# Optimization experiments

Hardware: AMD Instinct MI355X
Metric: run time of the kernel (lower is better)

Reference implementation:

```python
import jax, jax.numpy as jnp
import numpy as np
from jax import lax

C = 128
KS = 9
PAD = KS // 2


def _conv1d(r, w):
    # r: [B, C, L], w: [Cout, Cin, K] -> [B, C, L], SAME padding
    return lax.conv_general_dilated(r, w, window_strides=(1,), padding=[(PAD, PAD)],
                                    dimension_numbers=("NCH", "OIH", "NCH"))


def _pass_once(x, w, vertical, reverse):
    # x: [B, C, H, W]; scan sequentially along H (vertical) or W (horizontal).
    if not vertical:
        x = jnp.transpose(x, (0, 1, 3, 2))  # scan axis -> axis 2
    if reverse:
        x = jnp.flip(x, axis=2)
    xs = jnp.moveaxis(x, 2, 0)  # [S, B, C, L]

    def step(carry, xi):
        y = xi + jax.nn.relu(_conv1d(carry, w))
        return y, y

    _, ys = lax.scan(step, xs[0], xs[1:])
    out = jnp.concatenate([xs[:1], ys], axis=0)
    out = jnp.moveaxis(out, 0, 2)
    if reverse:
        out = jnp.flip(out, axis=2)
    if not vertical:
        out = jnp.transpose(out, (0, 1, 3, 2))
    return out


def setup_inputs() -> dict:
    key = jax.random.key(0)
    kx, k1, k2, k3, k4 = jax.random.split(key, 5)
    B, H, W = 8, 128, 256
    std = (1.0 / (C * KS)) ** 0.5  # kaiming_normal_(a=1) scale
    x = jax.random.normal(kx, (B, C, H, W), dtype=jnp.float32)
    w_ud = jax.random.normal(k1, (C, C, KS), dtype=jnp.float32) * std
    w_du = jax.random.normal(k2, (C, C, KS), dtype=jnp.float32) * std
    w_lr = jax.random.normal(k3, (C, C, KS), dtype=jnp.float32) * std
    w_rl = jax.random.normal(k4, (C, C, KS), dtype=jnp.float32) * std
    return {"x": x, "w_ud": w_ud, "w_du": w_du, "w_lr": w_lr, "w_rl": w_rl}


def reference(x, w_ud, w_du, w_lr, w_rl):
    # Order matches torch ModuleList: up_down, down_up, left_right, right_left
    x = _pass_once(x, w_ud, vertical=True, reverse=False)
    x = _pass_once(x, w_du, vertical=True, reverse=True)
    x = _pass_once(x, w_lr, vertical=False, reverse=False)
    x = _pass_once(x, w_rl, vertical=False, reverse=True)
    return x
```

## Files before the change

kernel.cpp:

```cpp
#include <hip/hip_runtime.h>

#define C_ 128
#define KS_ 9
#define B_ 8
#define H_ 128
#define W_ 256
#define HW_ (H_ * W_)
#define CHW_ (C_ * HW_)

typedef _Float16 half8 __attribute__((ext_vector_type(8)));
typedef float floatx4 __attribute__((ext_vector_type(4)));
typedef unsigned long long ull;

#define F16_IMG_BYTES 67108864u

#define WS_WF_OFF    0u
#define WS_WF_BYTES  1179648u
#define WS_CARRY_OFF 1183744u
#define CARRY_HALVES (8 * 256 * 128)
#define WS_YT_OFF    2232320u
#define WS_NEED      (WS_YT_OFF + F16_IMG_BYTES)

__device__ __forceinline__ int imin(int a, int b) { return a < b ? a : b; }
__device__ __forceinline__ int imax(int a, int b) { return a > b ? a : b; }

__global__ void k_copy(const float* __restrict__ in, float* __restrict__ out, int n4) {
  int i = blockIdx.x * blockDim.x + threadIdx.x;
  int stride = gridDim.x * blockDim.x;
  const floatx4* ip = (const floatx4*)in;
  floatx4* op = (floatx4*)out;
  for (; i < n4; i += stride) op[i] = ip[i];
}

__global__ void k_wprep(const float* w0, const float* w1, const float* w2, const float* w3,
                        _Float16* __restrict__ wf) {
  const float* Wp[4] = {w0, w1, w2, w3};
  const float* W = Wp[blockIdx.y];
  _Float16* out = wf + (size_t)blockIdx.y * (8 * 36 * 64 * 8);
  int idx = blockIdx.x * 256 + threadIdx.x;
  if (idx >= 8 * 36 * 64 * 8) return;
  int j = idx & 7;
  int lane = (idx >> 3) & 63;
  int ks = (idx >> 9) % 36;
  int mt = (idx >> 9) / 36;
  int co = mt * 16 + (lane & 15);
  int k = ks * 32 + ((lane >> 4) & 3) * 8 + j;
  int kk = k >> 7, ci = k & 127;
  out[idx] = (_Float16)W[((size_t)co * C_ + ci) * KS_ + kk];
}

template <typename XT, typename YT>
__global__ void k_carry0(const XT* __restrict__ imgX, YT* __restrict__ imgY,
                         _Float16* __restrict__ cout_, int S, int L, int istart) {
  int b = blockIdx.y;
  int e = blockIdx.x * 256 + threadIdx.x;
  if (e >= L * 16) return;
  int col = e >> 4, ci0 = (e & 15) * 8;
  union { ull u[2]; _Float16 h[8]; } pk;
#pragma unroll
  for (int u2 = 0; u2 < 8; ++u2) {
    size_t off = ((size_t)(b * C_ + ci0 + u2) * S + istart) * L + col;
    float v = (float)imgX[off];
    pk.h[u2] = (_Float16)v;
    imgY[off] = (YT)v;
  }
  ull* dst = (ull*)(cout_ + ((size_t)b * L + col) * 128 + ci0);
  dst[0] = pk.u[0];
  dst[1] = pk.u[1];
}

__global__ void k_t1h(const _Float16* __restrict__ in, _Float16* __restrict__ out) {
  __shared__ _Float16 tile[32][33];
  size_t pbase = (size_t)blockIdx.z * HW_;
  int h0 = blockIdx.y * 32, w0 = blockIdx.x * 32;
  int tx = threadIdx.x, ty = threadIdx.y;
  for (int i = 0; i < 32; i += 8)
    tile[ty + i][tx] = in[pbase + (size_t)(h0 + ty + i) * W_ + (w0 + tx)];
  __syncthreads();
  for (int i = 0; i < 32; i += 8)
    out[pbase + (size_t)(w0 + ty + i) * H_ + (h0 + tx)] = tile[tx][ty + i];
}

__global__ void k_t2(const _Float16* __restrict__ in, float* __restrict__ out) {
  __shared__ float tile[32][33];
  size_t pbase = (size_t)blockIdx.z * HW_;
  int h0 = blockIdx.y * 32, w0 = blockIdx.x * 32;
  int tx = threadIdx.x, ty = threadIdx.y;
  for (int i = 0; i < 32; i += 8)
    tile[ty + i][tx] = (float)in[pbase + (size_t)(w0 + ty + i) * H_ + (h0 + tx)];
  __syncthreads();
  for (int i = 0; i < 32; i += 8)
    out[pbase + (size_t)(h0 + ty + i) * W_ + (w0 + tx)] = tile[tx][ty + i];
}

template <typename XT, typename YT, int WC, int MAXT>
__global__ __launch_bounds__(512, 2) void k_scan3(
    const XT* __restrict__ imgX, YT* __restrict__ imgY,
    const _Float16* __restrict__ Wf, const _Float16* __restrict__ cin,
    _Float16* __restrict__ cout_,
    int S, int L, int n0, int nsteps, int dir, int istart) {
  constexpr int MAXW = WC + 72;
  constexpr int BSZ = MAXW * 132;
  __shared__ _Float16 Bl[2][BSZ];
  __shared__ floatx4 Sc[2][8][64];
  const int c0 = blockIdx.x * WC;
  const int b = blockIdx.y;
  const int t = threadIdx.x;
  const int lane = t & 63, wave = t >> 6;
  const int q = lane >> 4, m = lane & 15;
  const int h = wave & 1;
  const int g = wave >> 1;

  half8 A0[18], A1[18];
  {
    const half8* wp2 = (const half8*)Wf;
#pragma unroll
    for (int i = 0; i < 18; ++i) {
      A0[i] = wp2[((g * 2 + 0) * 36 + h * 18 + i) * 64 + lane];
      A1[i] = wp2[((g * 2 + 1) * 36 + h * 18 + i) * 64 + lane];
    }
  }

  for (int i = t * 8; i < BSZ; i += 4096) {
    ull* z0 = (ull*)(&Bl[0][i]);
    ull* z1 = (ull*)(&Bl[1][i]);
    z0[0] = 0ull; z0[1] = 0ull;
    z1[0] = 0ull; z1[1] = 0ull;
  }
  __syncthreads();

  {
    const int NCH = (WC + 64) * 16;
    for (int e = t; e < NCH; e += 512) {
      const int lcol = e >> 4;
      const int col = c0 - 32 + lcol;
      if (col >= 0 && col < L) {
        const int ci0 = (e & 15) * 8;
        const ull* src = (const ull*)(cin + ((size_t)b * L + col) * 128 + ci0);
        ull* dst = (ull*)(&Bl[0][(lcol + 4) * 132 + ci0]);
        dst[0] = src[0];
        dst[1] = src[1];
      }
    }
  }
  __syncthreads();

  int cur = 0;
  for (int p = 1; p <= nsteps; ++p) {
    const int row = istart + dir * (n0 + p);
    const int ext = 32 - 4 * p;
    const int lo = imax(c0 - ext, 0);
    const int hi = imin(c0 + WC + ext, L);
    const int tt0 = -((c0 - lo + 15) >> 4);
    const int ntile = ((hi - c0 + 15) >> 4) - tt0;
    const _Float16* BR = Bl[cur];
    _Float16* BW = Bl[cur ^ 1];
    const size_t rbase = ((size_t)(b * C_ + wave * 16) * S + row) * L;

    float xv[MAXT][4];
#pragma unroll
    for (int u = 0; u < MAXT; ++u) {
      if (u >= ntile) break;
      const int col = c0 + (tt0 + u) * 16 + m;
      const bool ld2 = (col >= lo) && (col < hi);
#pragma unroll
      for (int r = 0; r < 4; ++r)
        xv[u][r] = ld2 ? (float)imgX[rbase + (size_t)(q * 4 + r) * (S * L) + col] : 0.f;
    }

#pragma unroll
    for (int u = 0; u < MAXT; ++u) {
      if (u >= ntile) break;
      const int ti = tt0 + u;
      floatx4 aA = {0.f, 0.f, 0.f, 0.f}, aB = {0.f, 0.f, 0.f, 0.f};
      const int lbase = ti * 16 + m + 32;
#pragma unroll
      for (int i = 0; i < 18; ++i) {
        const int ks = h * 18 + i;
        const int kk = ks >> 2;
        const int ci0 = (ks & 3) * 32 + q * 8;
        const ull* bp = (const ull*)(BR + (lbase + kk) * 132 + ci0);
        union { ull u2[2]; half8 v; } bf;
        bf.u2[0] = bp[0]; bf.u2[1] = bp[1];
        aA = __builtin_amdgcn_mfma_f32_16x16x32_f16(A0[i], bf.v, aA, 0, 0, 0);
        aB = __builtin_amdgcn_mfma_f32_16x16x32_f16(A1[i], bf.v, aB, 0, 0, 0);
      }
      Sc[u & 1][wave][lane] = h ? aA : aB;
      __syncthreads();
      const floatx4 ac = (h ? aB : aA) + Sc[u & 1][wave ^ 1][lane];
      const int col = c0 + ti * 16 + m;
      const bool instrip = (col >= c0) && (col < c0 + WC);
      const bool inlds = (col >= lo) && (col < hi);
      union { ull uu; _Float16 h4[4]; } pk;
#pragma unroll
      for (int r = 0; r < 4; ++r) {
        const float y = xv[u][r] + fmaxf(ac[r], 0.f);
        pk.h4[r] = (_Float16)y;
        if (instrip)
          imgY[rbase + (size_t)(q * 4 + r) * (S * L) + col] = (YT)y;
      }
      if (inlds)
        *(ull*)(BW + (col - c0 + 36) * 132 + wave * 16 + q * 4) = pk.uu;
    }
    __syncthreads();
    cur ^= 1;
  }

  {
    const _Float16* BP = Bl[cur];
    for (int e = t; e < WC * 16; e += 512) {
      const int lc = e >> 4, ci0 = (e & 15) * 8;
      ull* dst = (ull*)(cout_ + ((size_t)b * L + (c0 + lc)) * 128 + ci0);
      const ull* src = (const ull*)(BP + (lc + 36) * 132 + ci0);
      dst[0] = src[0];
      dst[1] = src[1];
    }
  }
}

__device__ __forceinline__ void gemm_acc_fb(const _Float16* Bl, const _Float16* __restrict__ Wfrag,
                                            int wrow_base, int lane, floatx4* acc) {
  const int q = lane >> 4;
  const half8* wfp = (const half8*)Wfrag + lane;
  for (int ks = 0; ks < 36; ++ks) {
    int k0 = ks * 32 + q * 8;
    int kk = k0 >> 7;
    int ci0 = k0 & 127;
    half8 bf = *(const half8*)&Bl[(size_t)(wrow_base + kk) * C_ + ci0];
    const half8* wp = wfp + ks * 64;
#pragma unroll
    for (int mt = 0; mt < 8; ++mt)
      acc[mt] = __builtin_amdgcn_mfma_f32_16x16x32_f16(wp[mt * 36 * 64], bf, acc[mt], 0, 0, 0);
  }
}

__global__ __launch_bounds__(256) void k_step_v(float* __restrict__ Y,
                                                const _Float16* __restrict__ Wfrag,
                                                int row, int prev) {
  __shared__ _Float16 Bl[80 * 128];
  const int b = blockIdx.y, w0 = blockIdx.x * 64, t = threadIdx.x;
  {
    const float* base = Y + (size_t)b * CHW_ + (size_t)prev * W_;
#pragma unroll
    for (int it = 0; it < 10; ++it) {
      int c = it * 256 + t;
      int ci = c / 20, c4 = c % 20;
      int wst = w0 - 8 + c4 * 4;
      const float* p = base + (size_t)ci * HW_ + wst;
      float v[4];
      if (wst >= 0 && wst + 4 <= W_) {
        floatx4 u = *(const floatx4*)p;
        v[0] = u[0]; v[1] = u[1]; v[2] = u[2]; v[3] = u[3];
      } else {
#pragma unroll
        for (int j = 0; j < 4; ++j) { int w = wst + j; v[j] = (w >= 0 && w < W_) ? p[j] : 0.f; }
      }
      int wl = c4 * 4;
#pragma unroll
      for (int j = 0; j < 4; ++j) Bl[(wl + j) * C_ + ci] = (_Float16)v[j];
    }
  }
  __syncthreads();
  const int lane = t & 63, wave = t >> 6, q = lane >> 4, l15 = lane & 15;
  floatx4 acc[8];
#pragma unroll
  for (int mt = 0; mt < 8; ++mt) acc[mt] = (floatx4){0.f, 0.f, 0.f, 0.f};
  gemm_acc_fb(Bl, Wfrag, wave * 16 + l15 + 4, lane, acc);
  const int wcol = w0 + wave * 16 + l15;
#pragma unroll
  for (int mt = 0; mt < 8; ++mt)
#pragma unroll
    for (int r = 0; r < 4; ++r) {
      int co = mt * 16 + q * 4 + r;
      size_t off = (size_t)b * CHW_ + (size_t)co * HW_ + (size_t)row * W_ + wcol;
      Y[off] = Y[off] + fmaxf(acc[mt][r], 0.f);
    }
}

__global__ __launch_bounds__(256) void k_step_h(float* __restrict__ Y,
                                                const _Float16* __restrict__ Wfrag,
                                                int row, int prev) {
  __shared__ _Float16 Bl[80 * 128];
  const int b = blockIdx.y, h0 = blockIdx.x * 64, t = threadIdx.x;
  {
    const float* base = Y + (size_t)b * CHW_ + prev;
    for (int e = t; e < 80 * 128; e += 256) {
      int hl = e >> 7, ci = e & 127, h = h0 - 8 + hl;
      float v = 0.f;
      if (h >= 0 && h < H_) v = base[(size_t)ci * HW_ + (size_t)h * W_];
      Bl[hl * C_ + ci] = (_Float16)v;
    }
  }
  __syncthreads();
  const int lane = t & 63, wave = t >> 6, q = lane >> 4, l15 = lane & 15;
  floatx4 acc[8];
#pragma unroll
  for (int mt = 0; mt < 8; ++mt) acc[mt] = (floatx4){0.f, 0.f, 0.f, 0.f};
  gemm_acc_fb(Bl, Wfrag, wave * 16 + l15 + 4, lane, acc);
  const int hc = h0 + wave * 16 + l15;
#pragma unroll
  for (int mt = 0; mt < 8; ++mt)
#pragma unroll
    for (int r = 0; r < 4; ++r) {
      int co = mt * 16 + q * 4 + r;
      size_t off = (size_t)b * CHW_ + (size_t)co * HW_ + (size_t)hc * W_ + row;
      Y[off] = Y[off] + fmaxf(acc[mt][r], 0.f);
    }
}

extern "C" void kernel_launch(void* const* d_in, const int* in_sizes, int n_in,
                              void* d_out, int out_size, void* d_ws, size_t ws_size,
                              hipStream_t stream) {
  const float* x = (const float*)d_in[0];
  const float* w_ud = (const float*)d_in[1];
  const float* w_du = (const float*)d_in[2];
  const float* w_lr = (const float*)d_in[3];
  const float* w_rl = (const float*)d_in[4];

  float* Y = (float*)d_out;
  char* ws = (char*)d_ws;
  _Float16* Wf = (_Float16*)(ws + WS_WF_OFF);
  _Float16* carryA = (_Float16*)(ws + WS_CARRY_OFF);
  _Float16* carryB = carryA + CARRY_HALVES;
  _Float16* YtA = (_Float16*)(ws + WS_YT_OFF);
  _Float16* F16A = (_Float16*)d_out;
  _Float16* F16B = (_Float16*)((char*)d_out + F16_IMG_BYTES);

  const size_t WF_PASS = 8 * 36 * 64 * 8;

  k_wprep<<<dim3(576, 4), 256, 0, stream>>>(w_ud, w_du, w_lr, w_rl, Wf);

  if (ws_size >= WS_NEED) {
    _Float16* cb_[2] = {carryA, carryB};
    k_carry0<float, float><<<dim3(16, B_), 256, 0, stream>>>(x, Y, carryA, H_, W_, 0);
    for (int n0 = 0, j = 0; n0 < H_ - 1; n0 += 8, ++j) {
      int ns = H_ - 1 - n0; if (ns > 8) ns = 8;
      k_scan3<float, float, 8, 5><<<dim3(32, B_), 512, 0, stream>>>(
          x, Y, Wf + 0 * WF_PASS, cb_[j & 1], cb_[(j + 1) & 1], H_, W_, n0, ns, +1, 0);
    }
    k_carry0<float, _Float16><<<dim3(16, B_), 256, 0, stream>>>(Y, YtA, carryA, H_, W_, H_ - 1);
    for (int n0 = 0, j = 0; n0 < H_ - 1; n0 += 8, ++j) {
      int ns = H_ - 1 - n0; if (ns > 8) ns = 8;
      k_scan3<float, _Float16, 8, 5><<<dim3(32, B_), 512, 0, stream>>>(
          Y, YtA, Wf + 1 * WF_PASS, cb_[j & 1], cb_[(j + 1) & 1], H_, W_, n0, ns, -1, H_ - 1);
    }
    k_t1h<<<dim3(8, 4, B_ * C_), dim3(32, 8), 0, stream>>>(YtA, F16A);
    k_carry0<_Float16, _Float16><<<dim3(8, B_), 256, 0, stream>>>(F16A, YtA, carryA, W_, H_, 0);
    for (int n0 = 0, j = 0; n0 < W_ - 1; n0 += 8, ++j) {
      int ns = W_ - 1 - n0; if (ns > 8) ns = 8;
      k_scan3<_Float16, _Float16, 4, 5><<<dim3(32, B_), 512, 0, stream>>>(
          F16A, YtA, Wf + 2 * WF_PASS, cb_[j & 1], cb_[(j + 1) & 1], W_, H_, n0, ns, +1, 0);
    }
    k_carry0<_Float16, _Float16><<<dim3(8, B_), 256, 0, stream>>>(YtA, F16B, carryA, W_, H_, W_ - 1);
    for (int n0 = 0, j = 0; n0 < W_ - 1; n0 += 8, ++j) {
      int ns = W_ - 1 - n0; if (ns > 8) ns = 8;
      k_scan3<_Float16, _Float16, 4, 5><<<dim3(32, B_), 512, 0, stream>>>(
          YtA, F16B, Wf + 3 * WF_PASS, cb_[j & 1], cb_[(j + 1) & 1], W_, H_, n0, ns, -1, W_ - 1);
    }
    k_copy<<<2048, 256, 0, stream>>>((const float*)F16B, (float*)YtA, F16_IMG_BYTES / 16);
    k_t2<<<dim3(8, 4, B_ * C_), dim3(32, 8), 0, stream>>>(YtA, Y);
  } else {
    k_copy<<<2048, 256, 0, stream>>>(x, Y, B_ * C_ * H_ * W_ / 4);
    for (int i = 1; i < H_; ++i)
      k_step_v<<<dim3(W_ / 64, B_), 256, 0, stream>>>(Y, Wf + 0 * WF_PASS, i, i - 1);
    for (int i = H_ - 2; i >= 0; --i)
      k_step_v<<<dim3(W_ / 64, B_), 256, 0, stream>>>(Y, Wf + 1 * WF_PASS, i, i + 1);
    for (int i = 1; i < W_; ++i)
      k_step_h<<<dim3(H_ / 64, B_), 256, 0, stream>>>(Y, Wf + 2 * WF_PASS, i, i - 1);
    for (int i = W_ - 2; i >= 0; --i)
      k_step_h<<<dim3(H_ / 64, B_), 256, 0, stream>>>(Y, Wf + 3 * WF_PASS, i, i + 1);
  }
}
```

Baseline: 4.215 ms.

## Single-buffer LDS carry, batch tile syncs, prefetch next row inputs

The scan kernel moves from double-buffered LDS to a single buffer, with the row stride padded to 136. All MFMA tiles are computed before one barrier instead of syncing per tile, so the cross-wave partial sums now need one scratch slot per tile. The next row's x values are loaded before the end-of-step barrier so the global load latency overlaps the sync. MAXT drops to 4 for the horizontal passes to cut register and LDS use. The single buffer depends on every read finishing before the barrier that precedes the writes.

```diff
diff --git a/kernel.cpp b/kernel.cpp
--- a/kernel.cpp
+++ b/kernel.cpp
@@ -100,9 +100,9 @@
     _Float16* __restrict__ cout_,
     int S, int L, int n0, int nsteps, int dir, int istart) {
   constexpr int MAXW = WC + 72;
-  constexpr int BSZ = MAXW * 132;
-  __shared__ _Float16 Bl[2][BSZ];
-  __shared__ floatx4 Sc[2][8][64];
+  constexpr int BSZ = MAXW * 136;
+  __shared__ _Float16 Bl[BSZ];
+  __shared__ floatx4 Sc[MAXT][8][64];
   const int c0 = blockIdx.x * WC;
   const int b = blockIdx.y;
   const int t = threadIdx.x;
@@ -122,10 +122,9 @@
   }
 
   for (int i = t * 8; i < BSZ; i += 4096) {
-    ull* z0 = (ull*)(&Bl[0][i]);
-    ull* z1 = (ull*)(&Bl[1][i]);
-    z0[0] = 0ull; z0[1] = 0ull;
-    z1[0] = 0ull; z1[1] = 0ull;
+    ull* z = (ull*)(&Bl[i]);
+    z[0] = 0ull;
+    z[1] = 0ull;
   }
   __syncthreads();
 
@@ -137,27 +136,24 @@
       if (col >= 0 && col < L) {
         const int ci0 = (e & 15) * 8;
         const ull* src = (const ull*)(cin + ((size_t)b * L + col) * 128 + ci0);
-        ull* dst = (ull*)(&Bl[0][(lcol + 4) * 132 + ci0]);
+        ull* dst = (ull*)(&Bl[(lcol + 4) * 136 + ci0]);
         dst[0] = src[0];
         dst[1] = src[1];
       }
     }
   }
-  __syncthreads();
-
-  int cur = 0;
-  for (int p = 1; p <= nsteps; ++p) {
-    const int row = istart + dir * (n0 + p);
-    const int ext = 32 - 4 * p;
-    const int lo = imax(c0 - ext, 0);
-    const int hi = imin(c0 + WC + ext, L);
-    const int tt0 = -((c0 - lo + 15) >> 4);
-    const int ntile = ((hi - c0 + 15) >> 4) - tt0;
-    const _Float16* BR = Bl[cur];
-    _Float16* BW = Bl[cur ^ 1];
-    const size_t rbase = ((size_t)(b * C_ + wave * 16) * S + row) * L;
-
-    float xv[MAXT][4];
+
+  int row, lo, hi, tt0, ntile;
+  size_t rbase;
+  float xv[MAXT][4];
+  {
+    row = istart + dir * (n0 + 1);
+    const int ext = 32 - 4;
+    lo = imax(c0 - ext, 0);
+    hi = imin(c0 + WC + ext, L);
+    tt0 = -((c0 - lo + 15) >> 4);
+    ntile = ((hi - c0 + 15) >> 4) - tt0;
+    rbase = ((size_t)(b * C_ + wave * 16) * S + row) * L;
 #pragma unroll
     for (int u = 0; u < MAXT; ++u) {
       if (u >= ntile) break;
@@ -167,7 +163,11 @@
       for (int r = 0; r < 4; ++r)
         xv[u][r] = ld2 ? (float)imgX[rbase + (size_t)(q * 4 + r) * (S * L) + col] : 0.f;
     }
-
+  }
+  __syncthreads();
+
+  for (int p = 1; p <= nsteps; ++p) {
+    floatx4 xa[MAXT];
 #pragma unroll
     for (int u = 0; u < MAXT; ++u) {
       if (u >= ntile) break;
@@ -179,15 +179,20 @@
         const int ks = h * 18 + i;
         const int kk = ks >> 2;
         const int ci0 = (ks & 3) * 32 + q * 8;
-        const ull* bp = (const ull*)(BR + (lbase + kk) * 132 + ci0);
-        union { ull u2[2]; half8 v; } bf;
-        bf.u2[0] = bp[0]; bf.u2[1] = bp[1];
-        aA = __builtin_amdgcn_mfma_f32_16x16x32_f16(A0[i], bf.v, aA, 0, 0, 0);
-        aB = __builtin_amdgcn_mfma_f32_16x16x32_f16(A1[i], bf.v, aB, 0, 0, 0);
-      }
-      Sc[u & 1][wave][lane] = h ? aA : aB;
-      __syncthreads();
-      const floatx4 ac = (h ? aB : aA) + Sc[u & 1][wave ^ 1][lane];
+        const half8 bf = *(const half8*)(Bl + (lbase + kk) * 136 + ci0);
+        aA = __builtin_amdgcn_mfma_f32_16x16x32_f16(A0[i], bf, aA, 0, 0, 0);
+        aB = __builtin_amdgcn_mfma_f32_16x16x32_f16(A1[i], bf, aB, 0, 0, 0);
+      }
+      Sc[u][wave][lane] = h ? aA : aB;
+      xa[u] = h ? aB : aA;
+    }
+    __syncthreads();
+
+#pragma unroll
+    for (int u = 0; u < MAXT; ++u) {
+      if (u >= ntile) break;
+      const int ti = tt0 + u;
+      const floatx4 ac = xa[u] + Sc[u][wave ^ 1][lane];
       const int col = c0 + ti * 16 + m;
       const bool instrip = (col >= c0) && (col < c0 + WC);
       const bool inlds = (col >= lo) && (col < hi);
@@ -200,18 +205,35 @@
           imgY[rbase + (size_t)(q * 4 + r) * (S * L) + col] = (YT)y;
       }
       if (inlds)
-        *(ull*)(BW + (col - c0 + 36) * 132 + wave * 16 + q * 4) = pk.uu;
+        *(ull*)(Bl + (col - c0 + 36) * 136 + wave * 16 + q * 4) = pk.uu;
+    }
+
+    if (p < nsteps) {
+      row = istart + dir * (n0 + p + 1);
+      const int ext = 32 - 4 * (p + 1);
+      lo = imax(c0 - ext, 0);
+      hi = imin(c0 + WC + ext, L);
+      tt0 = -((c0 - lo + 15) >> 4);
+      ntile = ((hi - c0 + 15) >> 4) - tt0;
+      rbase = ((size_t)(b * C_ + wave * 16) * S + row) * L;
+#pragma unroll
+      for (int u = 0; u < MAXT; ++u) {
+        if (u >= ntile) break;
+        const int col = c0 + (tt0 + u) * 16 + m;
+        const bool ld2 = (col >= lo) && (col < hi);
+#pragma unroll
+        for (int r = 0; r < 4; ++r)
+          xv[u][r] = ld2 ? (float)imgX[rbase + (size_t)(q * 4 + r) * (S * L) + col] : 0.f;
+      }
     }
     __syncthreads();
-    cur ^= 1;
-  }
-
-  {
-    const _Float16* BP = Bl[cur];
+  }
+
+  {
     for (int e = t; e < WC * 16; e += 512) {
       const int lc = e >> 4, ci0 = (e & 15) * 8;
       ull* dst = (ull*)(cout_ + ((size_t)b * L + (c0 + lc)) * 128 + ci0);
-      const ull* src = (const ull*)(BP + (lc + 36) * 132 + ci0);
+      const ull* src = (const ull*)(Bl + (lc + 36) * 136 + ci0);
       dst[0] = src[0];
       dst[1] = src[1];
     }
@@ -348,13 +370,13 @@
     k_carry0<_Float16, _Float16><<<dim3(8, B_), 256, 0, stream>>>(F16A, YtA, carryA, W_, H_, 0);
     for (int n0 = 0, j = 0; n0 < W_ - 1; n0 += 8, ++j) {
       int ns = W_ - 1 - n0; if (ns > 8) ns = 8;
-      k_scan3<_Float16, _Float16, 4, 5><<<dim3(32, B_), 512, 0, stream>>>(
+      k_scan3<_Float16, _Float16, 4, 4><<<dim3(32, B_), 512, 0, stream>>>(
           F16A, YtA, Wf + 2 * WF_PASS, cb_[j & 1], cb_[(j + 1) & 1], W_, H_, n0, ns, +1, 0);
     }
     k_carry0<_Float16, _Float16><<<dim3(8, B_), 256, 0, stream>>>(YtA, F16B, carryA, W_, H_, W_ - 1);
     for (int n0 = 0, j = 0; n0 < W_ - 1; n0 += 8, ++j) {
       int ns = W_ - 1 - n0; if (ns > 8) ns = 8;
-      k_scan3<_Float16, _Float16, 4, 5><<<dim3(32, B_), 512, 0, stream>>>(
+      k_scan3<_Float16, _Float16, 4, 4><<<dim3(32, B_), 512, 0, stream>>>(
           YtA, F16B, Wf + 3 * WF_PASS, cb_[j & 1], cb_[(j + 1) & 1], W_, H_, n0, ns, -1, W_ - 1);
     }
     k_copy<<<2048, 256, 0, stream>>>((const float*)F16B, (float*)YtA, F16_IMG_BYTES / 16);
```

Result: no change. 4.161 ms (-1.3%).
